# Kernel optimization log

Hardware: AMD Instinct MI355X
Metric: run time of the kernel (lower is better)

## Reference

```python
import jax, jax.numpy as jnp
import numpy as np

# constants matching init_kwargs
CLASSES = 80
CONF_T = 0.05
IOU_T = 0.5
MAX_DET = 100
MAX_DET_PER_CLASS = 100


def setup_inputs() -> dict:
    key = jax.random.key(0)
    k1, k2, k3, k4 = jax.random.split(key, 4)
    B, N = 8, 2048
    # structured predictions: [x1, y1, x2, y2, class, score] in a 640x640 image
    xy1 = jax.random.uniform(k1, (B, N, 2), dtype=jnp.float32) * 580.0
    wh = jax.random.uniform(k2, (B, N, 2), dtype=jnp.float32) * 60.0 + 1.0
    cls = jax.random.randint(k3, (B, N), 0, CLASSES).astype(jnp.float32)
    sc = jax.random.uniform(k4, (B, N), dtype=jnp.float32)
    predictions = jnp.concatenate([xy1, xy1 + wh, cls[..., None], sc[..., None]], axis=-1)
    return {"predictions": predictions}


def _pairwise_iou(b):
    # b: [B, N, 4] xyxy (IoU is invariant under xyxy<->yxyx swap used by the layer)
    x1, y1, x2, y2 = b[..., 0], b[..., 1], b[..., 2], b[..., 3]
    area = jnp.maximum(x2 - x1, 0.0) * jnp.maximum(y2 - y1, 0.0)  # [B,N]
    ix1 = jnp.maximum(x1[:, :, None], x1[:, None, :])
    iy1 = jnp.maximum(y1[:, :, None], y1[:, None, :])
    ix2 = jnp.minimum(x2[:, :, None], x2[:, None, :])
    iy2 = jnp.minimum(y2[:, :, None], y2[:, None, :])
    inter = jnp.maximum(ix2 - ix1, 0.0) * jnp.maximum(iy2 - iy1, 0.0)  # [B,N,N]
    union = area[:, :, None] + area[:, None, :] - inter
    return inter / jnp.maximum(union, 1e-8)


def reference(predictions):
    # Combined per-class NMS. Because scores are one-hot over classes (score *
    # one_hot(class)), per-class NMS is equivalent to class-aware greedy NMS on
    # the globally score-sorted boxes where suppression only acts within a class.
    B, N, _ = predictions.shape
    boxes = predictions[..., :4]
    cls = predictions[..., 4].astype(jnp.int32)
    scores = predictions[..., 5]
    valid = scores > CONF_T

    # sort by score descending (invalid boxes pushed to the end)
    order = jnp.argsort(jnp.where(valid, scores, -jnp.inf), axis=1)[:, ::-1]  # [B,N]
    bsort = jnp.take_along_axis(boxes, order[..., None], axis=1)
    ssort = jnp.take_along_axis(scores, order, axis=1)
    csort = jnp.take_along_axis(cls, order, axis=1)
    vsort = jnp.take_along_axis(valid, order, axis=1)

    iou = _pairwise_iou(bsort)  # [B,N,N]
    same_cls = csort[:, :, None] == csort[:, None, :]
    sup_mat = same_cls & (iou > IOU_T)  # [B,N,N] bool

    idxs = jnp.arange(N)

    def body(i, keep):
        active = keep[:, i]  # [B] is box i still alive?
        sup = keep & sup_mat[:, i, :] & (idxs > i)[None, :]
        return jnp.where(active[:, None], keep & ~sup, keep)

    keep = jax.lax.fori_loop(0, N, body, vsort)  # [B,N]

    # per-class cap (max_detections_per_class): rank among kept boxes of same class
    oh = jax.nn.one_hot(csort, CLASSES, dtype=jnp.float32)  # [B,N,C]
    csum = jnp.cumsum(oh * keep[..., None].astype(jnp.float32), axis=1)
    rank = jnp.take_along_axis(csum, csort[..., None], axis=2)[..., 0]  # [B,N]
    keep = keep & (rank <= MAX_DET_PER_CLASS)

    # global top max_detections among kept boxes
    final = jnp.where(keep, ssort, -1.0)
    _, ti = jax.lax.top_k(final, MAX_DET)  # [B,MAX_DET]
    v = jnp.take_along_axis(keep, ti, axis=1)
    boxes_out = jnp.where(v[..., None], jnp.take_along_axis(bsort, ti[..., None], axis=1), 0.0)
    scores_out = jnp.where(v, jnp.take_along_axis(ssort, ti, axis=1), 0.0)
    classes_out = jnp.where(v, jnp.take_along_axis(csort, ti, axis=1).astype(jnp.float32), 0.0)
    num_det = jnp.sum(v, axis=1).astype(jnp.int32)
    return boxes_out, scores_out, classes_out, num_det
```

## Files before the change

kernel.cpp:

```cpp
#include <hip/hip_runtime.h>
#include <stdint.h>

#define NB 2048
#define NCLASSES 80
#define CONF_T 0.05f
#define IOU_T 0.5f
#define MAX_DET 100
#define MAX_PER_CLASS 100

typedef unsigned long long u64;
typedef unsigned int u32;
typedef unsigned char u8;

__device__ __forceinline__ u64 shfl_xor_u64(u64 v, int mask) {
    int lo = (int)(u32)v, hi = (int)(u32)(v >> 32);
    lo = __shfl_xor(lo, mask, 64);
    hi = __shfl_xor(hi, mask, 64);
    return ((u64)(u32)hi << 32) | (u32)lo;
}

__global__ __launch_bounds__(512) void k_work(const float* __restrict__ pred,
                                              u64* __restrict__ keysG,
                                              u8* __restrict__ supBytes) {
    const int bid = blockIdx.x, tid = threadIdx.x;
    const int lane = tid & 63, wave = tid >> 6;

    __shared__ __align__(16) char smem[49152];
    u64*    keys = (u64*)smem;
    float2* csS  = (float2*)smem;
    u64*    wkey = (u64*)(smem + 16384);
    float4* wb4  = (float4*)(smem + 20480);
    u64*    wm   = (u64*)(smem + 28672);
    u8*     fst  = (u8*)(smem + 32768);

    if (bid < 8) {
        const int b = bid;
        const float* P = pred + (size_t)b * NB * 6;

        const int sbase = wave * 256;
        const int iA = sbase + lane, iB = iA + 64, iC = iA + 128, iD = iA + 192;

        auto mkkey = [&](int i) -> u64 {
            float s = P[i * 6 + 5];
            return (s > CONF_T) ? (((u64)__float_as_uint(s) << 32) | (u32)i)
                                : (u64)(u32)i;
        };
        u64 A = mkkey(iA), Bv = mkkey(iB), C = mkkey(iC), D = mkkey(iD);

        auto loc = [&](u64& X, u64& Y, int ix, int k) {
            bool up = ((ix & k) == 0);
            u64 mx = X > Y ? X : Y, mn = X > Y ? Y : X;
            X = up ? mx : mn; Y = up ? mn : mx;
        };
        auto shf = [&](u64& V, int iv, int j, int k) {
            u64 p = shfl_xor_u64(V, j);
            bool low = ((lane & j) == 0);
            bool up  = ((iv & k) == 0);
            V = (low == up) ? (V > p ? V : p) : (V < p ? V : p);
        };
        auto tail = [&](int k, int jstart) {
            if (jstart >= 128) { loc(A, C, iA, k); loc(Bv, D, iB, k); }
            if (jstart >= 64)  { loc(A, Bv, iA, k); loc(C, D, iC, k); }
            for (int j = (jstart > 32 ? 32 : jstart); j >= 1; j >>= 1) {
                shf(A, iA, j, k); shf(Bv, iB, j, k); shf(C, iC, j, k); shf(D, iD, j, k);
            }
        };

        for (int k = 2; k <= 256; k <<= 1) tail(k, k >> 1);
        keys[iA] = A; keys[iB] = Bv; keys[iC] = C; keys[iD] = D;
        __syncthreads();

        for (int k = 512; k <= NB; k <<= 1) {
            for (int j = k >> 1; j >= 256; j >>= 1) {
                for (int pp = tid; pp < (NB >> 1); pp += 512) {
                    int i1 = ((pp & ~(j - 1)) << 1) | (pp & (j - 1));
                    int i2 = i1 + j;
                    bool up = ((i1 & k) == 0);
                    u64 a = keys[i1], c = keys[i2];
                    if (up ? (a < c) : (a > c)) { keys[i1] = c; keys[i2] = a; }
                }
                __syncthreads();
            }
            A = keys[iA]; Bv = keys[iB]; C = keys[iC]; D = keys[iD];
            tail(k, 128);
            keys[iA] = A; keys[iB] = Bv; keys[iC] = C; keys[iD] = D;
            __syncthreads();
        }

        for (int i = tid; i < NB; i += 512)
            keysG[(size_t)b * NB + i] = keys[i];
    } else {
        const int idx = bid - 8;
        const int b = idx / 10;
        const int c = (idx % 10) * 8 + wave;
        const float* P = pred + (size_t)b * NB * 6;
        u8* sb = supBytes + (size_t)b * NB;

        for (int i = tid; i < NB; i += 512)
            csS[i] = *reinterpret_cast<const float2*>(P + i * 6 + 4);
        __syncthreads();

        u64* wkeyW = wkey + wave * 64;
        float4* wb4W = wb4 + wave * 64;
        u64* wmW = wm + wave * 64;

        int cnt = 0;
        for (int base = 0; base < NB; base += 64) {
            int i = base + lane;
            float2 cs = csS[i];
            bool v = (cs.y > CONF_T) && ((int)cs.x == c);
            u64 m = __ballot(v);
            if (v) {
                int pos = cnt + __popcll(m & ((1ull << lane) - 1ull));
                if (pos < 64) {
                    float2 p01 = *reinterpret_cast<const float2*>(P + i * 6);
                    float2 p23 = *reinterpret_cast<const float2*>(P + i * 6 + 2);
                    wkeyW[pos] = ((u64)__float_as_uint(cs.y) << 32) | (u32)i;
                    wb4W[pos] = make_float4(p01.x, p01.y, p23.x, p23.y);
                }
            }
            cnt += __popcll(m);
        }
        __builtin_amdgcn_wave_barrier();

        if (cnt <= 64) {
            u64 mykey = 0ull; int orig = 0;
            float x1 = 0.f, y1 = 0.f, x2 = 0.f, y2 = 0.f, ar = 0.f;
            if (lane < cnt) {
                mykey = wkeyW[lane];
                orig = (int)(u32)mykey;
                float4 bx = wb4W[lane];
                x1 = bx.x; y1 = bx.y; x2 = bx.z; y2 = bx.w;
                ar = fmaxf(x2 - x1, 0.f) * fmaxf(y2 - y1, 0.f);
            }
            u64 mj = 0ull;
            if (lane < cnt) {
                for (int i = 0; i < cnt; ++i) {
                    u64 ki = wkeyW[i];
                    if (ki > mykey) {
                        float4 bi = wb4W[i];
                        float ari = fmaxf(bi.z - bi.x, 0.f) * fmaxf(bi.w - bi.y, 0.f);
                        float ix1 = fmaxf(bi.x, x1), iy1 = fmaxf(bi.y, y1);
                        float ix2 = fminf(bi.z, x2), iy2 = fminf(bi.w, y2);
                        float inter = fmaxf(ix2 - ix1, 0.f) * fmaxf(iy2 - iy1, 0.f);
                        float uni = ari + ar - inter;
                        if (inter / fmaxf(uni, 1e-8f) > IOU_T) mj |= 1ull << i;
                    }
                }
            }
            u64 conf = __ballot(mj != 0ull);
            bool sup = false;
            if (conf != 0ull) {
                u64 srcs = mj;
                #pragma unroll
                for (int d = 1; d < 64; d <<= 1) srcs |= shfl_xor_u64(srcs, d);
                wmW[lane] = mj;
                __builtin_amdgcn_wave_barrier();
                u64 Cset = srcs | conf;
                u64 keptS = 0ull, rem = Cset;
                while (rem) {
                    u64 t = rem, bestk = 0ull; int bi = -1;
                    while (t) {
                        int i = __ffsll(t) - 1; t &= t - 1;
                        u64 k = wkeyW[i];
                        if (k > bestk) { bestk = k; bi = i; }
                    }
                    rem &= ~(1ull << bi);
                    if ((wmW[bi] & keptS) == 0ull) keptS |= 1ull << bi;
                }
                sup = (mj & keptS) != 0ull;
            }
            if (lane < cnt) sb[orig] = sup ? 1 : 0;
        } else {
            volatile u8* vf = fst + wave * NB;
            for (int o = lane; o < NB; o += 64) vf[o] = 0;
            __builtin_amdgcn_wave_barrier();
            int keptCount = 0;
            for (;;) {
                u64 best = 0ull; int bo = -1;
                for (int o = lane; o < NB; o += 64) {
                    if (vf[o]) continue;
                    float2 cs = csS[o];
                    if (cs.y > CONF_T && (int)cs.x == c) {
                        u64 k = ((u64)__float_as_uint(cs.y) << 32) | (u32)o;
                        if (k > best) { best = k; bo = o; }
                    }
                }
                for (int d = 32; d >= 1; d >>= 1) {
                    u64 ob = shfl_xor_u64(best, d);
                    int obo = __shfl_xor(bo, d, 64);
                    if (ob > best) { best = ob; bo = obo; }
                }
                if (best == 0ull) break;
                keptCount++;
                int orig = (int)(u32)best;
                if (lane == 0) {
                    vf[orig] = 1;
                    sb[orig] = (keptCount > MAX_PER_CLASS) ? 1 : 0;
                }
                __builtin_amdgcn_wave_barrier();
                const float* q = P + orig * 6;
                float ax1 = q[0], ay1 = q[1], ax2 = q[2], ay2 = q[3];
                float aar = fmaxf(ax2 - ax1, 0.f) * fmaxf(ay2 - ay1, 0.f);
                for (int o = lane; o < NB; o += 64) {
                    if (vf[o]) continue;
                    float2 cs = csS[o];
                    if (cs.y > CONF_T && (int)cs.x == c) {
                        const float* q2 = P + o * 6;
                        float bx1 = q2[0], by1 = q2[1], bx2 = q2[2], by2 = q2[3];
                        float br = fmaxf(bx2 - bx1, 0.f) * fmaxf(by2 - by1, 0.f);
                        float ix1 = fmaxf(ax1, bx1), iy1 = fmaxf(ay1, by1);
                        float ix2 = fminf(ax2, bx2), iy2 = fminf(ay2, by2);
                        float inter = fmaxf(ix2 - ix1, 0.f) * fmaxf(iy2 - iy1, 0.f);
                        if (inter / fmaxf(aar + br - inter, 1e-8f) > IOU_T) {
                            vf[o] = 2;
                            sb[o] = 1;
                        }
                    }
                }
                __builtin_amdgcn_wave_barrier();
            }
        }
    }
}

__global__ __launch_bounds__(256) void k_out2(const float* __restrict__ pred,
                                              const u64* __restrict__ keysG,
                                              const u8* __restrict__ supBytes,
                                              float* __restrict__ out, int B) {
    const int b = blockIdx.x, tid = threadIdx.x;
    const int wave = tid >> 6, lane = tid & 63;
    __shared__ u32 smw[NB / 4];
    __shared__ u64 keptM[32];
    __shared__ int kcnt[32], kbase[32];

    const u32* sw = (const u32*)(supBytes + (size_t)b * NB);
    for (int i = tid; i < NB / 4; i += 256) smw[i] = sw[i];
    __syncthreads();

    const u64* kg = keysG + (size_t)b * NB;
    const float* P = pred + (size_t)b * NB * 6;

    for (int cc = wave; cc < 32; cc += 4) {
        u64 k = kg[cc * 64 + lane];
        int orig = (int)(u32)k;
        bool kp = ((k >> 32) != 0) &&
                  (((smw[orig >> 2] >> ((orig & 3) * 8)) & 0xFFu) == 0u);
        u64 m = __ballot(kp);
        if (lane == 0) { keptM[cc] = m; kcnt[cc] = __popcll(m); }
    }
    __syncthreads();
    if (tid < 32) {
        int s = 0;
        for (int c2 = 0; c2 < tid; ++c2) s += kcnt[c2];
        kbase[tid] = s;
    }
    __syncthreads();

    float* boxes_out   = out + (size_t)b * MAX_DET * 4;
    float* scores_out  = out + (size_t)B * MAX_DET * 4 + (size_t)b * MAX_DET;
    float* classes_out = out + (size_t)B * MAX_DET * 5 + (size_t)b * MAX_DET;
    float* numdet_out  = out + (size_t)B * MAX_DET * 6 + b;

    for (int cc = wave; cc < 32; cc += 4) {
        u64 m = keptM[cc];
        bool kp = (m >> lane) & 1ull;
        int pos = kbase[cc] + __popcll(m & ((1ull << lane) - 1ull));
        if (kp && pos < MAX_DET) {
            u64 k = kg[cc * 64 + lane];
            int orig = (int)(u32)k;
            const float* q = P + orig * 6;
            boxes_out[pos * 4 + 0] = q[0];
            boxes_out[pos * 4 + 1] = q[1];
            boxes_out[pos * 4 + 2] = q[2];
            boxes_out[pos * 4 + 3] = q[3];
            scores_out[pos]  = __uint_as_float((u32)(k >> 32));
            classes_out[pos] = q[4];
        }
    }
    int total = kbase[31] + kcnt[31];
    int nd = total < MAX_DET ? total : MAX_DET;
    for (int p = nd + tid; p < MAX_DET; p += 256) {
        boxes_out[p * 4 + 0] = 0.f;
        boxes_out[p * 4 + 1] = 0.f;
        boxes_out[p * 4 + 2] = 0.f;
        boxes_out[p * 4 + 3] = 0.f;
        scores_out[p]  = 0.f;
        classes_out[p] = 0.f;
    }
    if (tid == 0) *numdet_out = (float)nd;
}

__global__ __launch_bounds__(1024) void nms_fallback(const float* __restrict__ pred,
                                                     float* __restrict__ out, int B) {
    const int b = blockIdx.x, tid = threadIdx.x;
    __shared__ u64 keys[NB];
    __shared__ float bx1[NB], by1[NB], bx2[NB], by2[NB];
    __shared__ int kc[NB];
    __shared__ int cnt[NCLASSES];
    __shared__ int overflow;
    const float* P = pred + (size_t)b * NB * 6;
    for (int i = tid; i < NB; i += 1024) {
        float s = P[i * 6 + 5];
        keys[i] = (s > CONF_T) ? (((u64)__float_as_uint(s) << 32) | (uint32_t)i)
                               : (u64)(uint32_t)i;
    }
    __syncthreads();
    for (int k = 2; k <= NB; k <<= 1)
        for (int j = k >> 1; j > 0; j >>= 1) {
            for (int i = tid; i < NB; i += 1024) {
                int ixj = i ^ j;
                if (ixj > i) {
                    u64 a = keys[i], c = keys[ixj];
                    bool up = ((i & k) == 0);
                    if (up ? (a < c) : (a > c)) { keys[i] = c; keys[ixj] = a; }
                }
            }
            __syncthreads();
        }
    for (int i = tid; i < NB; i += 1024) {
        u64 k = keys[i];
        int orig = (int)(uint32_t)k;
        const float* q = P + orig * 6;
        bx1[i] = q[0]; by1[i] = q[1]; bx2[i] = q[2]; by2[i] = q[3];
        kc[i] = ((k >> 32) != 0) ? (int)q[4] : -1;
    }
    __syncthreads();
    bool dirty = false;
    for (int i = 0; i < NB - 1; ++i) {
        if (i == 0 || dirty) { __syncthreads(); dirty = false; }
        int ci = kc[i];
        if (ci < 0) continue;
        dirty = true;
        float x1i = bx1[i], y1i = by1[i], x2i = bx2[i], y2i = by2[i];
        float ai = fmaxf(x2i - x1i, 0.f) * fmaxf(y2i - y1i, 0.f);
        for (int j = i + 1 + tid; j < NB; j += 1024) {
            if (kc[j] != ci) continue;
            float ix1 = fmaxf(x1i, bx1[j]), iy1 = fmaxf(y1i, by1[j]);
            float ix2 = fminf(x2i, bx2[j]), iy2 = fminf(y2i, by2[j]);
            float inter = fmaxf(ix2 - ix1, 0.f) * fmaxf(iy2 - iy1, 0.f);
            float aj = fmaxf(bx2[j] - bx1[j], 0.f) * fmaxf(by2[j] - by1[j], 0.f);
            if (inter / fmaxf(ai + aj - inter, 1e-8f) > IOU_T) kc[j] = -1;
        }
    }
    __syncthreads();
    for (int i = tid; i < NCLASSES; i += 1024) cnt[i] = 0;
    if (tid == 0) overflow = 0;
    __syncthreads();
    for (int i = tid; i < NB; i += 1024) if (kc[i] >= 0) atomicAdd(&cnt[kc[i]], 1);
    __syncthreads();
    if (tid < NCLASSES && cnt[tid] > MAX_PER_CLASS) atomicOr(&overflow, 1);
    __syncthreads();
    if (overflow) {
        if (tid == 0) {
            for (int c = 0; c < NCLASSES; ++c) cnt[c] = 0;
            for (int i = 0; i < NB; ++i)
                if (kc[i] >= 0 && ++cnt[kc[i]] > MAX_PER_CLASS) kc[i] = -1;
        }
        __syncthreads();
    }
    if (tid < 64) {
        const int lane = tid;
        float* boxes_out   = out + (size_t)b * MAX_DET * 4;
        float* scores_out  = out + (size_t)B * MAX_DET * 4 + (size_t)b * MAX_DET;
        float* classes_out = out + (size_t)B * MAX_DET * 5 + (size_t)b * MAX_DET;
        float* numdet_out  = out + (size_t)B * MAX_DET * 6 + b;
        int running = 0;
        for (int chunk = 0; chunk < NB / 64; ++chunk) {
            int j = chunk * 64 + lane;
            int c = kc[j];
            bool k = (c >= 0);
            u64 m = __ballot(k);
            int pos = running + __popcll(m & ((1ull << lane) - 1ull));
            if (k && pos < MAX_DET) {
                boxes_out[pos * 4 + 0] = bx1[j];
                boxes_out[pos * 4 + 1] = by1[j];
                boxes_out[pos * 4 + 2] = bx2[j];
                boxes_out[pos * 4 + 3] = by2[j];
                scores_out[pos]  = __uint_as_float((uint32_t)(keys[j] >> 32));
                classes_out[pos] = (float)c;
            }
            running += __popcll(m);
        }
        int nd = running < MAX_DET ? running : MAX_DET;
        for (int p = nd + lane; p < MAX_DET; p += 64) {
            boxes_out[p * 4 + 0] = 0.f; boxes_out[p * 4 + 1] = 0.f;
            boxes_out[p * 4 + 2] = 0.f; boxes_out[p * 4 + 3] = 0.f;
            scores_out[p] = 0.f; classes_out[p] = 0.f;
        }
        if (lane == 0) *numdet_out = (float)nd;
    }
}

extern "C" void kernel_launch(void* const* d_in, const int* in_sizes, int n_in,
                              void* d_out, int out_size, void* d_ws, size_t ws_size,
                              hipStream_t stream) {
    const float* pred = (const float*)d_in[0];
    float* out = (float*)d_out;
    const int B = in_sizes[0] / (NB * 6);
    const size_t nBox = (size_t)B * NB;

    u64* keysG = (u64*)d_ws;
    u8* supBytes = (u8*)(keysG + nBox);
    const size_t need = nBox * 8 + nBox;

    if (B != 8 || ws_size < need) {
        nms_fallback<<<B, 1024, 0, stream>>>(pred, out, B);
        return;
    }

    k_work<<<8 + B * 10, 512, 0, stream>>>(pred, keysG, supBytes);
    k_out2<<<B, 256, 0, stream>>>(pred, keysG, supBytes, out, B);
}
```

Before: 27.09 us.

## Replace full score sort with histogram threshold selection of top candidates

Removes the 8 full 2048-element bitonic-sort blocks from the per-class kernel and drops the global keys buffer. The selection kernel now builds a 512-bucket histogram of surviving scores, finds a threshold bucket that holds the top 100, and bitonic-sorts only up to 256 candidates within one wave. If more than 256 candidates pass the threshold it falls back to a full shared-memory bitonic sort. This shifts sorting work off the critical first kernel at the cost of atomics and an extra histogram pass in the second kernel.

```diff
diff --git a/kernel.cpp b/kernel.cpp
--- a/kernel.cpp
+++ b/kernel.cpp
@@ -19,241 +19,272 @@
     return ((u64)(u32)hi << 32) | (u32)lo;
 }
 
-__global__ __launch_bounds__(512) void k_work(const float* __restrict__ pred,
-                                              u64* __restrict__ keysG,
-                                              u8* __restrict__ supBytes) {
-    const int bid = blockIdx.x, tid = threadIdx.x;
+__device__ __forceinline__ int sbucket(u32 bits) {
+    int b = (int)(bits >> 17) - 0x1E80;
+    return b < 0 ? 0 : (b > 511 ? 511 : b);
+}
+
+__global__ __launch_bounds__(512) void k_class(const float* __restrict__ pred,
+                                               u8* __restrict__ supBytes) {
+    const int idx = blockIdx.x, tid = threadIdx.x;
     const int lane = tid & 63, wave = tid >> 6;
 
     __shared__ __align__(16) char smem[49152];
-    u64*    keys = (u64*)smem;
     float2* csS  = (float2*)smem;
     u64*    wkey = (u64*)(smem + 16384);
     float4* wb4  = (float4*)(smem + 20480);
     u64*    wm   = (u64*)(smem + 28672);
     u8*     fst  = (u8*)(smem + 32768);
 
-    if (bid < 8) {
-        const int b = bid;
-        const float* P = pred + (size_t)b * NB * 6;
-
-        const int sbase = wave * 256;
-        const int iA = sbase + lane, iB = iA + 64, iC = iA + 128, iD = iA + 192;
-
-        auto mkkey = [&](int i) -> u64 {
-            float s = P[i * 6 + 5];
-            return (s > CONF_T) ? (((u64)__float_as_uint(s) << 32) | (u32)i)
-                                : (u64)(u32)i;
-        };
-        u64 A = mkkey(iA), Bv = mkkey(iB), C = mkkey(iC), D = mkkey(iD);
-
-        auto loc = [&](u64& X, u64& Y, int ix, int k) {
-            bool up = ((ix & k) == 0);
-            u64 mx = X > Y ? X : Y, mn = X > Y ? Y : X;
-            X = up ? mx : mn; Y = up ? mn : mx;
-        };
-        auto shf = [&](u64& V, int iv, int j, int k) {
-            u64 p = shfl_xor_u64(V, j);
-            bool low = ((lane & j) == 0);
-            bool up  = ((iv & k) == 0);
-            V = (low == up) ? (V > p ? V : p) : (V < p ? V : p);
-        };
-        auto tail = [&](int k, int jstart) {
-            if (jstart >= 128) { loc(A, C, iA, k); loc(Bv, D, iB, k); }
-            if (jstart >= 64)  { loc(A, Bv, iA, k); loc(C, D, iC, k); }
-            for (int j = (jstart > 32 ? 32 : jstart); j >= 1; j >>= 1) {
-                shf(A, iA, j, k); shf(Bv, iB, j, k); shf(C, iC, j, k); shf(D, iD, j, k);
-            }
-        };
-
-        for (int k = 2; k <= 256; k <<= 1) tail(k, k >> 1);
-        keys[iA] = A; keys[iB] = Bv; keys[iC] = C; keys[iD] = D;
+    const int b = idx / 10;
+    const int c = (idx % 10) * 8 + wave;
+    const float* P = pred + (size_t)b * NB * 6;
+    u8* sb = supBytes + (size_t)b * NB;
+
+    for (int i = tid; i < NB; i += 512)
+        csS[i] = *reinterpret_cast<const float2*>(P + i * 6 + 4);
+    __syncthreads();
+
+    u64* wkeyW = wkey + wave * 64;
+    float4* wb4W = wb4 + wave * 64;
+    u64* wmW = wm + wave * 64;
+
+    int cnt = 0;
+    for (int base = 0; base < NB; base += 64) {
+        int i = base + lane;
+        float2 cs = csS[i];
+        bool v = (cs.y > CONF_T) && ((int)cs.x == c);
+        u64 m = __ballot(v);
+        if (v) {
+            int pos = cnt + __popcll(m & ((1ull << lane) - 1ull));
+            if (pos < 64) {
+                float2 p01 = *reinterpret_cast<const float2*>(P + i * 6);
+                float2 p23 = *reinterpret_cast<const float2*>(P + i * 6 + 2);
+                wkeyW[pos] = ((u64)__float_as_uint(cs.y) << 32) | (u32)i;
+                wb4W[pos] = make_float4(p01.x, p01.y, p23.x, p23.y);
+            }
+        }
+        cnt += __popcll(m);
+    }
+    __builtin_amdgcn_wave_barrier();
+
+    if (cnt <= 64) {
+        u64 mykey = 0ull; int orig = 0;
+        float x1 = 0.f, y1 = 0.f, x2 = 0.f, y2 = 0.f, ar = 0.f;
+        if (lane < cnt) {
+            mykey = wkeyW[lane];
+            orig = (int)(u32)mykey;
+            float4 bx = wb4W[lane];
+            x1 = bx.x; y1 = bx.y; x2 = bx.z; y2 = bx.w;
+            ar = fmaxf(x2 - x1, 0.f) * fmaxf(y2 - y1, 0.f);
+        }
+        u64 mj = 0ull;
+        if (lane < cnt) {
+            for (int i = 0; i < cnt; ++i) {
+                u64 ki = wkeyW[i];
+                if (ki > mykey) {
+                    float4 bi = wb4W[i];
+                    float ari = fmaxf(bi.z - bi.x, 0.f) * fmaxf(bi.w - bi.y, 0.f);
+                    float ix1 = fmaxf(bi.x, x1), iy1 = fmaxf(bi.y, y1);
+                    float ix2 = fminf(bi.z, x2), iy2 = fminf(bi.w, y2);
+                    float inter = fmaxf(ix2 - ix1, 0.f) * fmaxf(iy2 - iy1, 0.f);
+                    float uni = ari + ar - inter;
+                    if (inter / fmaxf(uni, 1e-8f) > IOU_T) mj |= 1ull << i;
+                }
+            }
+        }
+        u64 conf = __ballot(mj != 0ull);
+        bool sup = false;
+        if (conf != 0ull) {
+            u64 srcs = mj;
+            #pragma unroll
+            for (int d = 1; d < 64; d <<= 1) srcs |= shfl_xor_u64(srcs, d);
+            wmW[lane] = mj;
+            __builtin_amdgcn_wave_barrier();
+            u64 Cset = srcs | conf;
+            u64 keptS2 = 0ull, rem = Cset;
+            while (rem) {
+                u64 t = rem, bestk = 0ull; int bi = -1;
+                while (t) {
+                    int i = __ffsll(t) - 1; t &= t - 1;
+                    u64 k = wkeyW[i];
+                    if (k > bestk) { bestk = k; bi = i; }
+                }
+                rem &= ~(1ull << bi);
+                if ((wmW[bi] & keptS2) == 0ull) keptS2 |= 1ull << bi;
+            }
+            sup = (mj & keptS2) != 0ull;
+        }
+        if (lane < cnt) sb[orig] = sup ? 1 : 0;
+    } else {
+        volatile u8* vf = fst + wave * NB;
+        for (int o = lane; o < NB; o += 64) vf[o] = 0;
+        __builtin_amdgcn_wave_barrier();
+        int keptCount = 0;
+        for (;;) {
+            u64 best = 0ull; int bo = -1;
+            for (int o = lane; o < NB; o += 64) {
+                if (vf[o]) continue;
+                float2 cs = csS[o];
+                if (cs.y > CONF_T && (int)cs.x == c) {
+                    u64 k = ((u64)__float_as_uint(cs.y) << 32) | (u32)o;
+                    if (k > best) { best = k; bo = o; }
+                }
+            }
+            for (int d = 32; d >= 1; d >>= 1) {
+                u64 ob = shfl_xor_u64(best, d);
+                int obo = __shfl_xor(bo, d, 64);
+                if (ob > best) { best = ob; bo = obo; }
+            }
+            if (best == 0ull) break;
+            keptCount++;
+            int orig = (int)(u32)best;
+            if (lane == 0) {
+                vf[orig] = 1;
+                sb[orig] = (keptCount > MAX_PER_CLASS) ? 1 : 0;
+            }
+            __builtin_amdgcn_wave_barrier();
+            const float* q = P + orig * 6;
+            float ax1 = q[0], ay1 = q[1], ax2 = q[2], ay2 = q[3];
+            float aar = fmaxf(ax2 - ax1, 0.f) * fmaxf(ay2 - ay1, 0.f);
+            for (int o = lane; o < NB; o += 64) {
+                if (vf[o]) continue;
+                float2 cs = csS[o];
+                if (cs.y > CONF_T && (int)cs.x == c) {
+                    const float* q2 = P + o * 6;
+                    float bx1 = q2[0], by1 = q2[1], bx2 = q2[2], by2 = q2[3];
+                    float br = fmaxf(bx2 - bx1, 0.f) * fmaxf(by2 - by1, 0.f);
+                    float ix1 = fmaxf(ax1, bx1), iy1 = fmaxf(ay1, by1);
+                    float ix2 = fminf(ax2, bx2), iy2 = fminf(ay2, by2);
+                    float inter = fmaxf(ix2 - ix1, 0.f) * fmaxf(iy2 - iy1, 0.f);
+                    if (inter / fmaxf(aar + br - inter, 1e-8f) > IOU_T) {
+                        vf[o] = 2;
+                        sb[o] = 1;
+                    }
+                }
+            }
+            __builtin_amdgcn_wave_barrier();
+        }
+    }
+}
+
+__global__ __launch_bounds__(256) void k_sel(const float* __restrict__ pred,
+                                             const u8* __restrict__ supBytes,
+                                             float* __restrict__ out, int B) {
+    const int b = blockIdx.x, tid = threadIdx.x;
+    __shared__ u32 smw[NB / 4];
+    __shared__ int hist[512];
+    __shared__ u64 cand[256];
+    __shared__ u64 skey[NB];
+    __shared__ int candCnt, TS, keptT;
+
+    const float* P = pred + (size_t)b * NB * 6;
+    const u32* sw = (const u32*)(supBytes + (size_t)b * NB);
+    for (int i = tid; i < NB / 4; i += 256) smw[i] = sw[i];
+    for (int i = tid; i < 512; i += 256) hist[i] = 0;
+    if (tid == 0) candCnt = 0;
+    __syncthreads();
+
+    u64 kreg[8];
+    #pragma unroll
+    for (int t = 0; t < 8; ++t) {
+        int i = tid + t * 256;
+        float s = P[i * 6 + 5];
+        bool sup = ((smw[i >> 2] >> ((i & 3) * 8)) & 0xFFu) != 0u;
+        u64 kk = 0ull;
+        if (s > CONF_T && !sup) {
+            u32 bits = __float_as_uint(s);
+            kk = ((u64)bits << 32) | (u32)i;
+            atomicAdd(&hist[sbucket(bits)], 1);
+        }
+        kreg[t] = kk;
+    }
+    __syncthreads();
+
+    if (tid < 64) {
+        int h[8], s = 0;
+        #pragma unroll
+        for (int t = 0; t < 8; ++t) { h[t] = hist[tid * 8 + t]; s += h[t]; }
+        int v = s;
+        #pragma unroll
+        for (int d = 1; d < 64; d <<= 1) {
+            int t2 = __shfl_down(v, d, 64);
+            if (tid + d < 64) v += t2;
+        }
+        int total = __shfl(v, 0, 64);
+        int target = total < MAX_DET ? total : MAX_DET;
+        int run = v - s, bestB = -1;
+        for (int t = 7; t >= 0; --t) {
+            run += h[t];
+            if (run >= target && bestB < 0) bestB = tid * 8 + t;
+        }
+        int T = bestB;
+        #pragma unroll
+        for (int d = 32; d >= 1; d >>= 1) {
+            int o = __shfl_xor(T, d, 64);
+            T = o > T ? o : T;
+        }
+        if (tid == 0) { TS = T; keptT = total; }
+    }
+    __syncthreads();
+
+    const int T = TS;
+    #pragma unroll
+    for (int t = 0; t < 8; ++t) {
+        u64 kk = kreg[t];
+        if (kk != 0ull && sbucket((u32)(kk >> 32)) >= T) {
+            int pos = atomicAdd(&candCnt, 1);
+            if (pos < 256) cand[pos] = kk;
+        }
+    }
+    __syncthreads();
+
+    int cc = candCnt;
+    if (cc <= 256) {
+        if (tid < 64) {
+            const int lane = tid;
+            const int iA = lane, iB = 64 + lane, iC = 128 + lane, iD = 192 + lane;
+            u64 A  = (iA < cc) ? cand[iA] : 0ull;
+            u64 Bv = (iB < cc) ? cand[iB] : 0ull;
+            u64 C  = (iC < cc) ? cand[iC] : 0ull;
+            u64 D  = (iD < cc) ? cand[iD] : 0ull;
+
+            auto loc = [&](u64& X, u64& Y, int ix, int k) {
+                bool up = ((ix & k) == 0);
+                u64 mx = X > Y ? X : Y, mn = X > Y ? Y : X;
+                X = up ? mx : mn; Y = up ? mn : mx;
+            };
+            auto shf = [&](u64& V, int iv, int j, int k) {
+                u64 p = shfl_xor_u64(V, j);
+                bool low = ((lane & j) == 0);
+                bool up  = ((iv & k) == 0);
+                V = (low == up) ? (V > p ? V : p) : (V < p ? V : p);
+            };
+            for (int k = 2; k <= 256; k <<= 1) {
+                int jstart = k >> 1;
+                if (jstart >= 128) { loc(A, C, iA, k); loc(Bv, D, iB, k); }
+                if (jstart >= 64)  { loc(A, Bv, iA, k); loc(C, D, iC, k); }
+                for (int j = (jstart > 32 ? 32 : jstart); j >= 1; j >>= 1) {
+                    shf(A, iA, j, k); shf(Bv, iB, j, k); shf(C, iC, j, k); shf(D, iD, j, k);
+                }
+            }
+            skey[iA] = A; skey[iB] = Bv; skey[iC] = C; skey[iD] = D;
+        }
+    } else {
+        #pragma unroll
+        for (int t = 0; t < 8; ++t) skey[tid + t * 256] = kreg[t];
         __syncthreads();
-
-        for (int k = 512; k <= NB; k <<= 1) {
-            for (int j = k >> 1; j >= 256; j >>= 1) {
-                for (int pp = tid; pp < (NB >> 1); pp += 512) {
+        for (int k = 2; k <= NB; k <<= 1)
+            for (int j = k >> 1; j > 0; j >>= 1) {
+                for (int pp = tid; pp < (NB >> 1); pp += 256) {
                     int i1 = ((pp & ~(j - 1)) << 1) | (pp & (j - 1));
                     int i2 = i1 + j;
                     bool up = ((i1 & k) == 0);
-                    u64 a = keys[i1], c = keys[i2];
-                    if (up ? (a < c) : (a > c)) { keys[i1] = c; keys[i2] = a; }
+                    u64 a = skey[i1], c2 = skey[i2];
+                    if (up ? (a < c2) : (a > c2)) { skey[i1] = c2; skey[i2] = a; }
                 }
                 __syncthreads();
             }
-            A = keys[iA]; Bv = keys[iB]; C = keys[iC]; D = keys[iD];
-            tail(k, 128);
-            keys[iA] = A; keys[iB] = Bv; keys[iC] = C; keys[iD] = D;
-            __syncthreads();
-        }
-
-        for (int i = tid; i < NB; i += 512)
-            keysG[(size_t)b * NB + i] = keys[i];
-    } else {
-        const int idx = bid - 8;
-        const int b = idx / 10;
-        const int c = (idx % 10) * 8 + wave;
-        const float* P = pred + (size_t)b * NB * 6;
-        u8* sb = supBytes + (size_t)b * NB;
-
-        for (int i = tid; i < NB; i += 512)
-            csS[i] = *reinterpret_cast<const float2*>(P + i * 6 + 4);
-        __syncthreads();
-
-        u64* wkeyW = wkey + wave * 64;
-        float4* wb4W = wb4 + wave * 64;
-        u64* wmW = wm + wave * 64;
-
-        int cnt = 0;
-        for (int base = 0; base < NB; base += 64) {
-            int i = base + lane;
-            float2 cs = csS[i];
-            bool v = (cs.y > CONF_T) && ((int)cs.x == c);
-            u64 m = __ballot(v);
-            if (v) {
-                int pos = cnt + __popcll(m & ((1ull << lane) - 1ull));
-                if (pos < 64) {
-                    float2 p01 = *reinterpret_cast<const float2*>(P + i * 6);
-                    float2 p23 = *reinterpret_cast<const float2*>(P + i * 6 + 2);
-                    wkeyW[pos] = ((u64)__float_as_uint(cs.y) << 32) | (u32)i;
-                    wb4W[pos] = make_float4(p01.x, p01.y, p23.x, p23.y);
-                }
-            }
-            cnt += __popcll(m);
-        }
-        __builtin_amdgcn_wave_barrier();
-
-        if (cnt <= 64) {
-            u64 mykey = 0ull; int orig = 0;
-            float x1 = 0.f, y1 = 0.f, x2 = 0.f, y2 = 0.f, ar = 0.f;
-            if (lane < cnt) {
-                mykey = wkeyW[lane];
-                orig = (int)(u32)mykey;
-                float4 bx = wb4W[lane];
-                x1 = bx.x; y1 = bx.y; x2 = bx.z; y2 = bx.w;
-                ar = fmaxf(x2 - x1, 0.f) * fmaxf(y2 - y1, 0.f);
-            }
-            u64 mj = 0ull;
-            if (lane < cnt) {
-                for (int i = 0; i < cnt; ++i) {
-                    u64 ki = wkeyW[i];
-                    if (ki > mykey) {
-                        float4 bi = wb4W[i];
-                        float ari = fmaxf(bi.z - bi.x, 0.f) * fmaxf(bi.w - bi.y, 0.f);
-                        float ix1 = fmaxf(bi.x, x1), iy1 = fmaxf(bi.y, y1);
-                        float ix2 = fminf(bi.z, x2), iy2 = fminf(bi.w, y2);
-                        float inter = fmaxf(ix2 - ix1, 0.f) * fmaxf(iy2 - iy1, 0.f);
-                        float uni = ari + ar - inter;
-                        if (inter / fmaxf(uni, 1e-8f) > IOU_T) mj |= 1ull << i;
-                    }
-                }
-            }
-            u64 conf = __ballot(mj != 0ull);
-            bool sup = false;
-            if (conf != 0ull) {
-                u64 srcs = mj;
-                #pragma unroll
-                for (int d = 1; d < 64; d <<= 1) srcs |= shfl_xor_u64(srcs, d);
-                wmW[lane] = mj;
-                __builtin_amdgcn_wave_barrier();
-                u64 Cset = srcs | conf;
-                u64 keptS = 0ull, rem = Cset;
-                while (rem) {
-                    u64 t = rem, bestk = 0ull; int bi = -1;
-                    while (t) {
-                        int i = __ffsll(t) - 1; t &= t - 1;
-                        u64 k = wkeyW[i];
-                        if (k > bestk) { bestk = k; bi = i; }
-                    }
-                    rem &= ~(1ull << bi);
-                    if ((wmW[bi] & keptS) == 0ull) keptS |= 1ull << bi;
-                }
-                sup = (mj & keptS) != 0ull;
-            }
-            if (lane < cnt) sb[orig] = sup ? 1 : 0;
-        } else {
-            volatile u8* vf = fst + wave * NB;
-            for (int o = lane; o < NB; o += 64) vf[o] = 0;
-            __builtin_amdgcn_wave_barrier();
-            int keptCount = 0;
-            for (;;) {
-                u64 best = 0ull; int bo = -1;
-                for (int o = lane; o < NB; o += 64) {
-                    if (vf[o]) continue;
-                    float2 cs = csS[o];
-                    if (cs.y > CONF_T && (int)cs.x == c) {
-                        u64 k = ((u64)__float_as_uint(cs.y) << 32) | (u32)o;
-                        if (k > best) { best = k; bo = o; }
-                    }
-                }
-                for (int d = 32; d >= 1; d >>= 1) {
-                    u64 ob = shfl_xor_u64(best, d);
-                    int obo = __shfl_xor(bo, d, 64);
-                    if (ob > best) { best = ob; bo = obo; }
-                }
-                if (best == 0ull) break;
-                keptCount++;
-                int orig = (int)(u32)best;
-                if (lane == 0) {
-                    vf[orig] = 1;
-                    sb[orig] = (keptCount > MAX_PER_CLASS) ? 1 : 0;
-                }
-                __builtin_amdgcn_wave_barrier();
-                const float* q = P + orig * 6;
-                float ax1 = q[0], ay1 = q[1], ax2 = q[2], ay2 = q[3];
-                float aar = fmaxf(ax2 - ax1, 0.f) * fmaxf(ay2 - ay1, 0.f);
-                for (int o = lane; o < NB; o += 64) {
-                    if (vf[o]) continue;
-                    float2 cs = csS[o];
-                    if (cs.y > CONF_T && (int)cs.x == c) {
-                        const float* q2 = P + o * 6;
-                        float bx1 = q2[0], by1 = q2[1], bx2 = q2[2], by2 = q2[3];
-                        float br = fmaxf(bx2 - bx1, 0.f) * fmaxf(by2 - by1, 0.f);
-                        float ix1 = fmaxf(ax1, bx1), iy1 = fmaxf(ay1, by1);
-                        float ix2 = fminf(ax2, bx2), iy2 = fminf(ay2, by2);
-                        float inter = fmaxf(ix2 - ix1, 0.f) * fmaxf(iy2 - iy1, 0.f);
-                        if (inter / fmaxf(aar + br - inter, 1e-8f) > IOU_T) {
-                            vf[o] = 2;
-                            sb[o] = 1;
-                        }
-                    }
-                }
-                __builtin_amdgcn_wave_barrier();
-            }
-        }
-    }
-}
-
-__global__ __launch_bounds__(256) void k_out2(const float* __restrict__ pred,
-                                              const u64* __restrict__ keysG,
-                                              const u8* __restrict__ supBytes,
-                                              float* __restrict__ out, int B) {
-    const int b = blockIdx.x, tid = threadIdx.x;
-    const int wave = tid >> 6, lane = tid & 63;
-    __shared__ u32 smw[NB / 4];
-    __shared__ u64 keptM[32];
-    __shared__ int kcnt[32], kbase[32];
-
-    const u32* sw = (const u32*)(supBytes + (size_t)b * NB);
-    for (int i = tid; i < NB / 4; i += 256) smw[i] = sw[i];
-    __syncthreads();
-
-    const u64* kg = keysG + (size_t)b * NB;
-    const float* P = pred + (size_t)b * NB * 6;
-
-    for (int cc = wave; cc < 32; cc += 4) {
-        u64 k = kg[cc * 64 + lane];
-        int orig = (int)(u32)k;
-        bool kp = ((k >> 32) != 0) &&
-                  (((smw[orig >> 2] >> ((orig & 3) * 8)) & 0xFFu) == 0u);
-        u64 m = __ballot(kp);
-        if (lane == 0) { keptM[cc] = m; kcnt[cc] = __popcll(m); }
-    }
-    __syncthreads();
-    if (tid < 32) {
-        int s = 0;
-        for (int c2 = 0; c2 < tid; ++c2) s += kcnt[c2];
-        kbase[tid] = s;
     }
     __syncthreads();
 
@@ -262,31 +293,26 @@
     float* classes_out = out + (size_t)B * MAX_DET * 5 + (size_t)b * MAX_DET;
     float* numdet_out  = out + (size_t)B * MAX_DET * 6 + b;
 
-    for (int cc = wave; cc < 32; cc += 4) {
-        u64 m = keptM[cc];
-        bool kp = (m >> lane) & 1ull;
-        int pos = kbase[cc] + __popcll(m & ((1ull << lane) - 1ull));
-        if (kp && pos < MAX_DET) {
-            u64 k = kg[cc * 64 + lane];
-            int orig = (int)(u32)k;
+    int nd = keptT < MAX_DET ? keptT : MAX_DET;
+    if (tid < MAX_DET) {
+        if (tid < nd) {
+            u64 kk = skey[tid];
+            int orig = (int)(u32)kk;
             const float* q = P + orig * 6;
-            boxes_out[pos * 4 + 0] = q[0];
-            boxes_out[pos * 4 + 1] = q[1];
-            boxes_out[pos * 4 + 2] = q[2];
-            boxes_out[pos * 4 + 3] = q[3];
-            scores_out[pos]  = __uint_as_float((u32)(k >> 32));
-            classes_out[pos] = q[4];
-        }
-    }
-    int total = kbase[31] + kcnt[31];
-    int nd = total < MAX_DET ? total : MAX_DET;
-    for (int p = nd + tid; p < MAX_DET; p += 256) {
-        boxes_out[p * 4 + 0] = 0.f;
-        boxes_out[p * 4 + 1] = 0.f;
-        boxes_out[p * 4 + 2] = 0.f;
-        boxes_out[p * 4 + 3] = 0.f;
-        scores_out[p]  = 0.f;
-        classes_out[p] = 0.f;
+            boxes_out[tid * 4 + 0] = q[0];
+            boxes_out[tid * 4 + 1] = q[1];
+            boxes_out[tid * 4 + 2] = q[2];
+            boxes_out[tid * 4 + 3] = q[3];
+            scores_out[tid]  = __uint_as_float((u32)(kk >> 32));
+            classes_out[tid] = q[4];
+        } else {
+            boxes_out[tid * 4 + 0] = 0.f;
+            boxes_out[tid * 4 + 1] = 0.f;
+            boxes_out[tid * 4 + 2] = 0.f;
+            boxes_out[tid * 4 + 3] = 0.f;
+            scores_out[tid]  = 0.f;
+            classes_out[tid] = 0.f;
+        }
     }
     if (tid == 0) *numdet_out = (float)nd;
 }
@@ -398,17 +424,15 @@
     const float* pred = (const float*)d_in[0];
     float* out = (float*)d_out;
     const int B = in_sizes[0] / (NB * 6);
-    const size_t nBox = (size_t)B * NB;
-
-    u64* keysG = (u64*)d_ws;
-    u8* supBytes = (u8*)(keysG + nBox);
-    const size_t need = nBox * 8 + nBox;
+
+    u8* supBytes = (u8*)d_ws;
+    const size_t need = (size_t)B * NB;
 
     if (B != 8 || ws_size < need) {
         nms_fallback<<<B, 1024, 0, stream>>>(pred, out, B);
         return;
     }
 
-    k_work<<<8 + B * 10, 512, 0, stream>>>(pred, keysG, supBytes);
-    k_out2<<<B, 256, 0, stream>>>(pred, keysG, supBytes, out, B);
-}
+    k_class<<<B * 10, 512, 0, stream>>>(pred, supBytes);
+    k_sel<<<B, 256, 0, stream>>>(pred, supBytes, out, B);
+}
```

New measurement: 29.82 us. +10.1%, slower.
